# Kernel optimization log

Measured on AMD Instinct MI355X. Metric: run time of the kernel, lower is better.

Reference implementation:

```python
import jax, jax.numpy as jnp
import numpy as np

B, P, C, D, H = 32, 2048, 19, 512, 4
DH = D // H  # 128
EPS = 1e-5


def setup_inputs() -> dict:
    key = jax.random.key(0)
    ks = jax.random.split(key, 12)
    s = 0.02
    return {
        "x": jax.random.normal(ks[0], (B, P, D), jnp.float32),
        "channel_embeddings": jax.random.normal(ks[1], (C, D), jnp.float32),
        "Wq": jax.random.normal(ks[2], (D, D), jnp.float32) * s,
        "bq": jnp.zeros((D,), jnp.float32),
        "Wk": jax.random.normal(ks[3], (D, D), jnp.float32) * s,
        "bk": jnp.zeros((D,), jnp.float32),
        "Wv": jax.random.normal(ks[4], (D, D), jnp.float32) * s,
        "bv": jnp.zeros((D,), jnp.float32),
        "Wo": jax.random.normal(ks[5], (D, D), jnp.float32) * s,
        "bo": jnp.zeros((D,), jnp.float32),
        "gamma": jnp.ones((D,), jnp.float32),
        "beta": jnp.zeros((D,), jnp.float32),
    }


def reference(x, channel_embeddings, Wq, bq, Wk, bk, Wv, bv, Wo, bo, gamma, beta):
    # q: (B, P, H, DH)
    q = (x @ Wq.T + bq).reshape(B, P, H, DH)
    # K/V depend only on channel embeddings (same for every batch/patch in the
    # original; it merely materialized the broadcast). Compute once: (C, H, DH)
    k = (channel_embeddings @ Wk.T + bk).reshape(C, H, DH)
    v = (channel_embeddings @ Wv.T + bv).reshape(C, H, DH)
    # scores over channels: (B, P, C, H)
    scores = jnp.einsum("bphd,chd->bpch", q, k) / jnp.sqrt(jnp.float32(DH))
    weights = jax.nn.softmax(scores, axis=2)  # softmax over channel dim
    # weighted sum of channel values: (B, P, H, DH) -> (B, P, D)
    attended = jnp.einsum("bpch,chd->bphd", weights, v).reshape(B, P, D)
    out = attended @ Wo.T + bo  # dropout is identity in eval mode
    # residual + layernorm
    h = x + out
    mean = jnp.mean(h, axis=-1, keepdims=True)
    var = jnp.mean(jnp.square(h - mean), axis=-1, keepdims=True)
    return (h - mean) * jax.lax.rsqrt(var + EPS) * gamma + beta
```

## Files before the change

kernel.cpp:

```cpp
#include <hip/hip_runtime.h>
#include <hip/hip_bf16.h>

#define C_  19
#define D_  512
#define H_  4
#define DH_ 128
#define NROW 65536
#define CHP_ 96

typedef float f32x4 __attribute__((ext_vector_type(4)));
typedef short bf16x8 __attribute__((ext_vector_type(8)));

__device__ __forceinline__ unsigned short f2bf(float f) {
  union { __hip_bfloat16 h; unsigned short s; } u;
  u.h = __float2bfloat16(f);
  return u.s;
}
__device__ __forceinline__ float bf2f(unsigned short h) {
  return __uint_as_float(((unsigned int)h) << 16);
}
__device__ __forceinline__ bf16x8 ld_cvt8(const float* p) {
  f32x4 v0 = *(const f32x4*)p;
  f32x4 v1 = *(const f32x4*)(p + 4);
  bf16x8 a;
  a[0]=(short)f2bf(v0[0]); a[1]=(short)f2bf(v0[1]);
  a[2]=(short)f2bf(v0[2]); a[3]=(short)f2bf(v0[3]);
  a[4]=(short)f2bf(v1[0]); a[5]=(short)f2bf(v1[1]);
  a[6]=(short)f2bf(v1[2]); a[7]=(short)f2bf(v1[3]);
  return a;
}

__global__ __launch_bounds__(512) void prep(
    const float* __restrict__ ce,
    const float* __restrict__ Wq, const float* __restrict__ bq,
    const float* __restrict__ Wk, const float* __restrict__ bk,
    const float* __restrict__ Wv, const float* __restrict__ bv,
    const float* __restrict__ Wo, const float* __restrict__ bo,
    unsigned short* __restrict__ Mtf, unsigned short* __restrict__ Utf,
    float* __restrict__ s0g)
{
  __shared__ float KV[2][DH_];
  __shared__ float KVp[512];

  const int p = blockIdx.x;
  const int m = threadIdx.x;
  const int mt_off = (p>>4)*8192 + (m>>5)*512 + ((((m>>3)&3)<<4) + (p&15))*8 + (m&7);
  const int ut_off = ((m>>4)*3 + (p>>5))*512 + ((((p>>3)&3)<<4) + (m&15))*8 + (p&7);
  const int c = p >> 2, h = p & 3;

  if (c >= C_) {
    if (p < 80) { Mtf[mt_off] = 0; if (m == 0) s0g[p] = 0.f; }
    Utf[ut_off] = (p == 80) ? f2bf(bo[m]) : (unsigned short)0;
    return;
  }

  {
    const int which = m >> 8;
    const int dh    = (m >> 1) & 127;
    const int half  = m & 1;
    const float* w = (which ? Wv : Wk) + (size_t)(h*DH_ + dh)*D_ + half*256;
    const float* e = ce + (size_t)c*D_ + half*256;
    float acc = 0.f;
    #pragma unroll 8
    for (int d = 0; d < 256; ++d) acc = fmaf(e[d], w[d], acc);
    KVp[m] = acc;
  }
  __syncthreads();
  if (m < 256) {
    const int which = m >> 7, dh = m & 127;
    KV[which][dh] = KVp[2*m] + KVp[2*m+1] + (which ? bv : bk)[h*DH_ + dh];
  }
  __syncthreads();

  const float rs128 = 0.08838834764831843f;
  float macc = 0.f;
  #pragma unroll 4
  for (int dh = 0; dh < DH_; ++dh)
    macc = fmaf(Wq[(size_t)(h*DH_+dh)*D_ + m], KV[0][dh], macc);
  Mtf[mt_off] = f2bf(macc * rs128);

  float uacc = 0.f;
  const float* wor = Wo + (size_t)m*D_ + h*DH_;
  #pragma unroll 4
  for (int dh = 0; dh < DH_; ++dh)
    uacc = fmaf(wor[dh], KV[1][dh], uacc);
  Utf[ut_off] = f2bf(uacc);

  if (m == 0) {
    float sa = 0.f;
    for (int dh = 0; dh < DH_; ++dh) sa = fmaf(bq[h*DH_+dh], KV[0][dh], sa);
    s0g[p] = sa * rs128;
  }
}

__global__ __launch_bounds__(256) void fused64(
    const float* __restrict__ x,
    const unsigned short* __restrict__ Mtf,
    const unsigned short* __restrict__ Utf,
    const float* __restrict__ s0g,
    const float* __restrict__ gamma, const float* __restrict__ beta,
    float* __restrict__ out)
{
  __shared__ __attribute__((aligned(16))) unsigned short Xbf[64*512];
  __shared__ __attribute__((aligned(16))) unsigned short WaL[64][104];
  __shared__ float rs_[64][2], rq_[64][2];

  const int t    = threadIdx.x;
  const int wave = t >> 6;
  const int lane = t & 63;
  const int lhi  = lane >> 4;
  const int llo  = lane & 15;
  const int row0 = blockIdx.x * 64;
  const int wrow = wave * 16;

  {
    #pragma unroll
    for (int j = 0; j < 16; ++j) {
      bf16x8 a = ld_cvt8(x + (size_t)(row0 + wrow + j)*D_ + lane*8);
      int byteoff = (wrow + j)*1024 + ((lane*16) ^ ((j & 7) << 4));
      *(bf16x8*)((char*)Xbf + byteoff) = a;
    }
  }
  asm volatile("s_waitcnt lgkmcnt(0)" ::: "memory");
  __builtin_amdgcn_sched_barrier(0);

  {
    const char* xb = (const char*)Xbf + (wrow + llo)*1024;
    const int swz = (llo & 7) << 4;
    f32x4 acc0 = (f32x4){0,0,0,0}, acc1 = acc0, acc2 = acc0, acc3 = acc0, acc4 = acc0;
    #pragma unroll
    for (int ks = 0; ks < 16; ++ks) {
      bf16x8 a = *(const bf16x8*)(xb + ((ks*64 + lhi*16) ^ swz));
      acc0 = __builtin_amdgcn_mfma_f32_16x16x32_bf16(a, *(const bf16x8*)(Mtf + 0*8192 + ks*512 + lane*8), acc0, 0, 0, 0);
      acc1 = __builtin_amdgcn_mfma_f32_16x16x32_bf16(a, *(const bf16x8*)(Mtf + 1*8192 + ks*512 + lane*8), acc1, 0, 0, 0);
      acc2 = __builtin_amdgcn_mfma_f32_16x16x32_bf16(a, *(const bf16x8*)(Mtf + 2*8192 + ks*512 + lane*8), acc2, 0, 0, 0);
      acc3 = __builtin_amdgcn_mfma_f32_16x16x32_bf16(a, *(const bf16x8*)(Mtf + 3*8192 + ks*512 + lane*8), acc3, 0, 0, 0);
      acc4 = __builtin_amdgcn_mfma_f32_16x16x32_bf16(a, *(const bf16x8*)(Mtf + 4*8192 + ks*512 + lane*8), acc4, 0, 0, 0);
    }
    const bool dead = (llo >= 12);
    float s0v0 = s0g[llo], s0v1 = s0g[16+llo], s0v2 = s0g[32+llo],
          s0v3 = s0g[48+llo], s0v4 = s0g[64+llo];
    #pragma unroll
    for (int r = 0; r < 4; ++r) {
      float v0 = acc0[r] + s0v0;
      float v1 = acc1[r] + s0v1;
      float v2 = acc2[r] + s0v2;
      float v3 = acc3[r] + s0v3;
      float v4 = dead ? -1e30f : (acc4[r] + s0v4);
      float mx = fmaxf(fmaxf(fmaxf(v0, v1), fmaxf(v2, v3)), v4);
      mx = fmaxf(mx, __shfl_xor(mx, 4, 64));
      mx = fmaxf(mx, __shfl_xor(mx, 8, 64));
      float e0 = __expf(v0 - mx), e1 = __expf(v1 - mx), e2 = __expf(v2 - mx),
            e3 = __expf(v3 - mx), e4 = dead ? 0.f : __expf(v4 - mx);
      float sm = e0 + e1 + e2 + e3 + e4;
      sm += __shfl_xor(sm, 4, 64);
      sm += __shfl_xor(sm, 8, 64);
      float inv = 1.f / sm;
      int lr = wrow + lhi*4 + r;
      WaL[lr][     llo] = f2bf(e0 * inv);
      WaL[lr][16 + llo] = f2bf(e1 * inv);
      WaL[lr][32 + llo] = f2bf(e2 * inv);
      WaL[lr][48 + llo] = f2bf(e3 * inv);
      WaL[lr][64 + llo] = f2bf(e4 * inv);
    }
    {
      int prow = wrow + lhi*4 + (llo & 3);
      int cj   = llo >> 2;
      WaL[prow][80 + cj*4 + 0] = (cj == 0) ? (unsigned short)0x3F80 : (unsigned short)0;
      WaL[prow][80 + cj*4 + 1] = 0;
      WaL[prow][80 + cj*4 + 2] = 0;
      WaL[prow][80 + cj*4 + 3] = 0;
    }
  }
  __syncthreads();

  const int rg = wave >> 1;
  const int cs = wave & 1;
  #pragma unroll
  for (int ha = 0; ha < 2; ++ha) {
    const int hrow = ha * 32;
    f32x4 oacc[16];
    #pragma unroll
    for (int i = 0; i < 16; ++i) oacc[i] = (f32x4){0.f,0.f,0.f,0.f};
    #pragma unroll
    for (int ks = 0; ks < 3; ++ks) {
      bf16x8 a = *(const bf16x8*)&WaL[hrow + rg*16 + llo][ks*32 + lhi*8];
      #pragma unroll
      for (int tile = 0; tile < 16; ++tile) {
        int ntile = cs*16 + tile;
        bf16x8 b = *(const bf16x8*)(Utf + (size_t)(ntile*3 + ks)*512 + lane*8);
        oacc[tile] = __builtin_amdgcn_mfma_f32_16x16x32_bf16(a, b, oacc[tile], 0, 0, 0);
      }
    }

    float s[4] = {0,0,0,0}, q[4] = {0,0,0,0};
    #pragma unroll
    for (int tile = 0; tile < 16; ++tile) {
      int n = cs*256 + tile*16 + llo;
      #pragma unroll
      for (int r = 0; r < 4; ++r) {
        int m = hrow + rg*16 + lhi*4 + r;
        float xres = bf2f(*(const unsigned short*)
            ((const char*)Xbf + m*1024 + ((n*2) ^ ((m & 7) << 4))));
        float val = oacc[tile][r] + xres;
        oacc[tile][r] = val;
        s[r] += val;
        q[r] = fmaf(val, val, q[r]);
      }
    }
    #pragma unroll
    for (int r = 0; r < 4; ++r) {
      #pragma unroll
      for (int off = 1; off < 16; off <<= 1) {
        s[r] += __shfl_xor(s[r], off, 64);
        q[r] += __shfl_xor(q[r], off, 64);
      }
    }
    if (llo == 0) {
      #pragma unroll
      for (int r = 0; r < 4; ++r) {
        rs_[hrow + rg*16 + lhi*4 + r][cs] = s[r];
        rq_[hrow + rg*16 + lhi*4 + r][cs] = q[r];
      }
    }
    __syncthreads();
    float mu_r[4], rstd_r[4];
    #pragma unroll
    for (int r = 0; r < 4; ++r) {
      int m = hrow + rg*16 + lhi*4 + r;
      float sum = rs_[m][0] + rs_[m][1];
      float sq  = rq_[m][0] + rq_[m][1];
      float mu  = sum * (1.f/(float)D_);
      float var = sq * (1.f/(float)D_) - mu*mu;
      mu_r[r]   = mu;
      rstd_r[r] = rsqrtf(var + 1e-5f);
    }
    #pragma unroll
    for (int tile = 0; tile < 16; ++tile) {
      int n = cs*256 + tile*16 + llo;
      float g = gamma[n], bt = beta[n];
      #pragma unroll
      for (int r = 0; r < 4; ++r) {
        int m = hrow + rg*16 + lhi*4 + r;
        out[(size_t)(row0 + m)*D_ + n] = (oacc[tile][r] - mu_r[r]) * rstd_r[r] * g + bt;
      }
    }
  }
}

extern "C" void kernel_launch(void* const* d_in, const int* in_sizes, int n_in,
                              void* d_out, int out_size, void* d_ws, size_t ws_size,
                              hipStream_t stream) {
  const float* x     = (const float*)d_in[0];
  const float* ce    = (const float*)d_in[1];
  const float* Wq    = (const float*)d_in[2];
  const float* bq    = (const float*)d_in[3];
  const float* Wk    = (const float*)d_in[4];
  const float* bk    = (const float*)d_in[5];
  const float* Wv    = (const float*)d_in[6];
  const float* bv    = (const float*)d_in[7];
  const float* Wo    = (const float*)d_in[8];
  const float* bo    = (const float*)d_in[9];
  const float* gamma = (const float*)d_in[10];
  const float* beta  = (const float*)d_in[11];
  float* out = (float*)d_out;

  char* ws = (char*)d_ws;
  unsigned short* Mtf = (unsigned short*)(ws);
  unsigned short* Utf = (unsigned short*)(ws + 81920);
  float* s0g          = (float*)(ws + 180224);

  prep<<<CHP_, 512, 0, stream>>>(ce, Wq, bq, Wk, bk, Wv, bv, Wo, bo,
                                 Mtf, Utf, s0g);
  fused64<<<NROW/64, 256, 0, stream>>>(x, Mtf, Utf, s0g, gamma, beta, out);
}
```

Baseline: 131.7 us.

## Transpose output MFMA so each wave owns its rows, drop cross-wave LayerNorm sync

The output projection MFMA now swaps operands (U as A, softmax weights as B), so each lane holds one row's outputs. Each wave computes all 512 columns for its own 16 rows instead of splitting columns across two waves. LayerNorm statistics then reduce with two shuffles, and the shared-memory partial buffers and block barriers go away. The first half of the results is kept packed as bf16 in registers to limit register pressure, and the fp32 output is written with vectorized 16-byte stores. The cost is an extra bf16 rounding of half the pre-norm values, and each wave reads the full U matrix.

```diff
diff --git a/kernel.cpp b/kernel.cpp
--- a/kernel.cpp
+++ b/kernel.cpp
@@ -10,6 +10,7 @@
 
 typedef float f32x4 __attribute__((ext_vector_type(4)));
 typedef short bf16x8 __attribute__((ext_vector_type(8)));
+typedef unsigned short ushort4v __attribute__((ext_vector_type(4)));
 
 __device__ __forceinline__ unsigned short f2bf(float f) {
   union { __hip_bfloat16 h; unsigned short s; } u;
@@ -103,7 +104,6 @@
 {
   __shared__ __attribute__((aligned(16))) unsigned short Xbf[64*512];
   __shared__ __attribute__((aligned(16))) unsigned short WaL[64][104];
-  __shared__ float rs_[64][2], rq_[64][2];
 
   const int t    = threadIdx.x;
   const int wave = t >> 6;
@@ -172,79 +172,101 @@
       WaL[prow][80 + cj*4 + 3] = 0;
     }
   }
-  __syncthreads();
-
-  const int rg = wave >> 1;
-  const int cs = wave & 1;
-  #pragma unroll
-  for (int ha = 0; ha < 2; ++ha) {
-    const int hrow = ha * 32;
-    f32x4 oacc[16];
-    #pragma unroll
-    for (int i = 0; i < 16; ++i) oacc[i] = (f32x4){0.f,0.f,0.f,0.f};
-    #pragma unroll
-    for (int ks = 0; ks < 3; ++ks) {
-      bf16x8 a = *(const bf16x8*)&WaL[hrow + rg*16 + llo][ks*32 + lhi*8];
-      #pragma unroll
-      for (int tile = 0; tile < 16; ++tile) {
-        int ntile = cs*16 + tile;
-        bf16x8 b = *(const bf16x8*)(Utf + (size_t)(ntile*3 + ks)*512 + lane*8);
-        oacc[tile] = __builtin_amdgcn_mfma_f32_16x16x32_bf16(a, b, oacc[tile], 0, 0, 0);
-      }
-    }
-
-    float s[4] = {0,0,0,0}, q[4] = {0,0,0,0};
-    #pragma unroll
-    for (int tile = 0; tile < 16; ++tile) {
-      int n = cs*256 + tile*16 + llo;
-      #pragma unroll
-      for (int r = 0; r < 4; ++r) {
-        int m = hrow + rg*16 + lhi*4 + r;
-        float xres = bf2f(*(const unsigned short*)
-            ((const char*)Xbf + m*1024 + ((n*2) ^ ((m & 7) << 4))));
-        float val = oacc[tile][r] + xres;
-        oacc[tile][r] = val;
-        s[r] += val;
-        q[r] = fmaf(val, val, q[r]);
-      }
-    }
+  asm volatile("s_waitcnt lgkmcnt(0)" ::: "memory");
+  __builtin_amdgcn_sched_barrier(0);
+
+  const int myrow = wrow + llo;
+  const char* xrow = (const char*)Xbf + myrow*1024;
+  const int rswz = (myrow & 7) << 4;
+  float s = 0.f, q = 0.f;
+  unsigned int pk[32];
+
+  f32x4 oa[16];
+  #pragma unroll
+  for (int i = 0; i < 16; ++i) oa[i] = (f32x4){0,0,0,0};
+  #pragma unroll
+  for (int ks = 0; ks < 3; ++ks) {
+    bf16x8 wb = *(const bf16x8*)&WaL[myrow][ks*32 + lhi*8];
+    #pragma unroll
+    for (int tl = 0; tl < 16; ++tl) {
+      bf16x8 ua = *(const bf16x8*)(Utf + (size_t)(tl*3 + ks)*512 + lane*8);
+      oa[tl] = __builtin_amdgcn_mfma_f32_16x16x32_bf16(ua, wb, oa[tl], 0, 0, 0);
+    }
+  }
+  #pragma unroll
+  for (int tl = 0; tl < 16; ++tl) {
+    ushort4v xr = *(const ushort4v*)(xrow + ((tl*32 + lhi*8) ^ rswz));
     #pragma unroll
     for (int r = 0; r < 4; ++r) {
-      #pragma unroll
-      for (int off = 1; off < 16; off <<= 1) {
-        s[r] += __shfl_xor(s[r], off, 64);
-        q[r] += __shfl_xor(q[r], off, 64);
-      }
-    }
-    if (llo == 0) {
-      #pragma unroll
-      for (int r = 0; r < 4; ++r) {
-        rs_[hrow + rg*16 + lhi*4 + r][cs] = s[r];
-        rq_[hrow + rg*16 + lhi*4 + r][cs] = q[r];
-      }
-    }
-    __syncthreads();
-    float mu_r[4], rstd_r[4];
+      float val = oa[tl][r] + bf2f(xr[r]);
+      oa[tl][r] = val;
+      s += val;
+      q = fmaf(val, val, q);
+    }
+    pk[tl*2    ] = (unsigned int)f2bf(oa[tl][0]) | ((unsigned int)f2bf(oa[tl][1]) << 16);
+    pk[tl*2 + 1] = (unsigned int)f2bf(oa[tl][2]) | ((unsigned int)f2bf(oa[tl][3]) << 16);
+  }
+
+  #pragma unroll
+  for (int i = 0; i < 16; ++i) oa[i] = (f32x4){0,0,0,0};
+  #pragma unroll
+  for (int ks = 0; ks < 3; ++ks) {
+    bf16x8 wb = *(const bf16x8*)&WaL[myrow][ks*32 + lhi*8];
+    #pragma unroll
+    for (int tl = 0; tl < 16; ++tl) {
+      bf16x8 ua = *(const bf16x8*)(Utf + (size_t)((16 + tl)*3 + ks)*512 + lane*8);
+      oa[tl] = __builtin_amdgcn_mfma_f32_16x16x32_bf16(ua, wb, oa[tl], 0, 0, 0);
+    }
+  }
+  #pragma unroll
+  for (int tl = 0; tl < 16; ++tl) {
+    ushort4v xr = *(const ushort4v*)(xrow + (((16 + tl)*32 + lhi*8) ^ rswz));
     #pragma unroll
     for (int r = 0; r < 4; ++r) {
-      int m = hrow + rg*16 + lhi*4 + r;
-      float sum = rs_[m][0] + rs_[m][1];
-      float sq  = rq_[m][0] + rq_[m][1];
-      float mu  = sum * (1.f/(float)D_);
-      float var = sq * (1.f/(float)D_) - mu*mu;
-      mu_r[r]   = mu;
-      rstd_r[r] = rsqrtf(var + 1e-5f);
-    }
-    #pragma unroll
-    for (int tile = 0; tile < 16; ++tile) {
-      int n = cs*256 + tile*16 + llo;
-      float g = gamma[n], bt = beta[n];
-      #pragma unroll
-      for (int r = 0; r < 4; ++r) {
-        int m = hrow + rg*16 + lhi*4 + r;
-        out[(size_t)(row0 + m)*D_ + n] = (oacc[tile][r] - mu_r[r]) * rstd_r[r] * g + bt;
-      }
-    }
+      float val = oa[tl][r] + bf2f(xr[r]);
+      oa[tl][r] = val;
+      s += val;
+      q = fmaf(val, val, q);
+    }
+  }
+
+  s += __shfl_xor(s, 16, 64);
+  s += __shfl_xor(s, 32, 64);
+  q += __shfl_xor(q, 16, 64);
+  q += __shfl_xor(q, 32, 64);
+  float mu   = s * (1.f/(float)D_);
+  float var  = q * (1.f/(float)D_) - mu*mu;
+  float rstd = rsqrtf(var + 1e-5f);
+
+  float* orow = out + (size_t)(row0 + myrow)*D_;
+  #pragma unroll
+  for (int tl = 0; tl < 16; ++tl) {
+    int n0 = tl*16 + lhi*4;
+    f32x4 gv = *(const f32x4*)(gamma + n0);
+    f32x4 bv = *(const f32x4*)(beta + n0);
+    float v0 = bf2f((unsigned short)(pk[tl*2] & 0xFFFF));
+    float v1 = bf2f((unsigned short)(pk[tl*2] >> 16));
+    float v2 = bf2f((unsigned short)(pk[tl*2+1] & 0xFFFF));
+    float v3 = bf2f((unsigned short)(pk[tl*2+1] >> 16));
+    f32x4 o;
+    o[0] = (v0 - mu) * rstd * gv[0] + bv[0];
+    o[1] = (v1 - mu) * rstd * gv[1] + bv[1];
+    o[2] = (v2 - mu) * rstd * gv[2] + bv[2];
+    o[3] = (v3 - mu) * rstd * gv[3] + bv[3];
+    *(f32x4*)(orow + n0) = o;
+  }
+  #pragma unroll
+  for (int tl = 0; tl < 16; ++tl) {
+    int n0 = 256 + tl*16 + lhi*4;
+    f32x4 gv = *(const f32x4*)(gamma + n0);
+    f32x4 bv = *(const f32x4*)(beta + n0);
+    f32x4 val = oa[tl];
+    f32x4 o;
+    o[0] = (val[0] - mu) * rstd * gv[0] + bv[0];
+    o[1] = (val[1] - mu) * rstd * gv[1] + bv[1];
+    o[2] = (val[2] - mu) * rstd * gv[2] + bv[2];
+    o[3] = (val[3] - mu) * rstd * gv[3] + bv[3];
+    *(f32x4*)(orow + n0) = o;
   }
 }
 
```

Result: slower. 145.5 us (+10.5%).
